# Performance work log

Measured on AMD Instinct MI355X. Metric: run time of the kernel, lower is better.

Reference implementation:

```python
import jax, jax.numpy as jnp
import numpy as np

B, C, T, H, W, E, K = 2, 256, 16, 32, 32, 4, 2


def setup_inputs() -> dict:
    key = jax.random.key(0)
    ks = jax.random.split(key, 5)
    x = jax.random.normal(ks[0], (B, C, T, H, W), dtype=jnp.float32)
    # gate: Conv3d(dim, E, 1) -> weight [E, C], bias [E]
    gate_w = jax.random.normal(ks[1], (E, C), dtype=jnp.float32) * 0.02
    gate_b = jnp.zeros((E,), dtype=jnp.float32)
    # experts_layer1: Conv3d(dim, dim*E, 1) -> weight [E*C, C], bias [E*C]
    w1 = jax.random.normal(ks[2], (E * C, C), dtype=jnp.float32) * 0.02
    b1 = jnp.zeros((E * C,), dtype=jnp.float32)
    # experts_layer2: Conv3d(dim*E, dim*E, 1, groups=E) -> per-expert [C, C]
    w2 = jax.random.normal(ks[3], (E, C, C), dtype=jnp.float32) * 0.02
    b2 = jnp.zeros((E, C), dtype=jnp.float32)
    return {"x": x, "gate_w": gate_w, "gate_b": gate_b,
            "w1": w1, "b1": b1, "w2": w2, "b2": b2}


def reference(x, gate_w, gate_b, w1, b1, w2, b2):
    # gating: 1x1x1 conv == channel contraction; logits [B,T,H,W,E]
    logits = jnp.einsum('bcthw,ec->bthwe', x, gate_w) + gate_b
    vals, idx = jax.lax.top_k(logits, K)              # [B,T,H,W,K]
    wk = jax.nn.softmax(vals, axis=-1).astype(x.dtype)
    # scatter top-k softmax weights back into E slots (zeros elsewhere)
    weights = jnp.sum(jax.nn.one_hot(idx, E, dtype=x.dtype) * wk[..., None],
                      axis=-2)                        # [B,T,H,W,E]
    # layer1 (dense 1x1x1 conv) + SiLU; output channels = E*C
    h = jax.nn.silu(jnp.einsum('bcthw,oc->bothw', x, w1)
                    + b1[None, :, None, None, None])
    h = h.reshape(B, E, C, T, H, W)
    # layer2: grouped 1x1x1 conv, one [C,C] matmul per expert
    expert_out = (jnp.einsum('becthw,eoc->beothw', h, w2)
                  + b2[None, :, :, None, None, None])  # [B,E,C,T,H,W]
    # weighted combine over experts + residual
    out = jnp.einsum('becthw,bthwe->bcthw', expert_out, weights)
    return out + x
```

## Files before the change

### kernel.cpp

```cpp
#include <hip/hip_runtime.h>
#include <hip/hip_bf16.h>


#define C_DIM 256
#define S_DIM 16384
#define E_DIM 4
#define MT 64
#define XST 264
#define OST 68
#define WFRAG_ELEMS 262144

typedef __attribute__((ext_vector_type(8))) short bf16x8;
typedef __attribute__((ext_vector_type(4))) short short4v;
typedef __attribute__((ext_vector_type(4))) float f32x4;

__device__ __forceinline__ short bfq(float f) {
  __hip_bfloat16 h = __float2bfloat16(f);
  return *(short*)&h;
}

__global__ __launch_bounds__(256) void prepack_kernel(
    const float* __restrict__ w1, const float* __restrict__ w2,
    __hip_bfloat16* __restrict__ dst)
{
  int o = blockIdx.x * 256 + threadIdx.x;
  int half = o >> 18;
  int idx = o & (WFRAG_ELEMS - 1);
  int j    = idx & 7;
  int lane = (idx >> 3) & 63;
  int kc   = (idx >> 9) & 7;
  int nt   = (idx >> 12) & 15;
  int e    = (idx >> 16) & 3;
  const float* src = half ? w2 : w1;
  int si = (e*256 + nt*16 + (lane & 15))*256 + kc*32 + (lane >> 4)*8 + j;
  dst[o] = __float2bfloat16(src[si]);
}

template<int MTC>
__device__ __forceinline__ void gemm1_sparse(
    const short* XsS, short* HsS, const short* w1e, const float* b1e,
    const unsigned char* plist_e, const float* wgtg_e,
    int wv, int r, int q)
{
  f32x4 hacc[MTC][2];
#pragma unroll
  for (int i = 0; i < MTC; ++i)
#pragma unroll
    for (int j = 0; j < 2; ++j) hacc[i][j] = (f32x4){0.f, 0.f, 0.f, 0.f};

  int aoff[MTC];
#pragma unroll
  for (int Mt = 0; Mt < MTC; ++Mt)
    aoff[Mt] = (int)plist_e[Mt*16 + r] * XST;

  bf16x8 bw[2][2];
#pragma unroll
  for (int t = 0; t < 2; ++t) bw[0][t] = *(const bf16x8*)(w1e + (t*8 + 0)*512);
#pragma unroll
  for (int kc = 0; kc < 8; ++kc) {
    if (kc < 7) {
#pragma unroll
      for (int t = 0; t < 2; ++t)
        bw[(kc+1)&1][t] = *(const bf16x8*)(w1e + (t*8 + kc + 1)*512);
    }
    bf16x8 a[MTC];
#pragma unroll
    for (int Mt = 0; Mt < MTC; ++Mt)
      a[Mt] = *(const bf16x8*)(XsS + aoff[Mt] + kc*32 + q*8);
#pragma unroll
    for (int Mt = 0; Mt < MTC; ++Mt)
#pragma unroll
      for (int t = 0; t < 2; ++t)
        hacc[Mt][t] = __builtin_amdgcn_mfma_f32_16x16x32_bf16(a[Mt], bw[kc&1][t], hacc[Mt][t], 0, 0, 0);
  }

#pragma unroll
  for (int Mt = 0; Mt < MTC; ++Mt) {
    const int g0 = Mt*16 + q*4;
    const unsigned pw = *(const unsigned*)(plist_e + g0);
    const f32x4 wg = *(const f32x4*)(wgtg_e + g0);
#pragma unroll
    for (int t = 0; t < 2; ++t) {
      const int n = wv*32 + t*16 + r;
      const float bias = b1e[n];
#pragma unroll
      for (int reg = 0; reg < 4; ++reg) {
        const int p = (pw >> (8*reg)) & 255;
        const float z = hacc[Mt][t][reg] + bias;
        const float s = __builtin_amdgcn_rcpf(1.0f + __expf(-z));
        HsS[p*XST + n] = bfq(z * s * wg[reg]);
      }
    }
  }
}

__global__ __launch_bounds__(512, 4) void moe_fused_kernel(
    const float* __restrict__ x,
    const float* __restrict__ gate_w,
    const float* __restrict__ gate_b,
    const float* __restrict__ b1,
    const float* __restrict__ b2,
    const __hip_bfloat16* __restrict__ wp,
    float* __restrict__ out)
{
  __shared__ __align__(16) char pool[256 * OST * 4];
  __shared__ float Wgt[MT * 4];
  __shared__ double GateP[512];
  __shared__ __align__(16) unsigned char plist[4][64];
  __shared__ __align__(16) float WgtG[4][64];
  __shared__ __align__(4)  unsigned char zlist[4][64];
  __shared__ int mcnt[4];

  short* XsS = (short*)pool;
  short* HsS = (short*)(pool + MT * XST * 2);
  float* Os  = (float*)pool;

  const int tid  = threadIdx.x;
  const int lane = tid & 63;
  const int wv   = tid >> 6;
  const int r    = lane & 15;
  const int q    = lane >> 4;

  const int g  = blockIdx.x;
  const int b  = g >> 8;
  const int s0 = (g & 255) * MT;
  const float* xb = x + (size_t)b * C_DIM * S_DIM + s0;

  {
    const int p4 = (tid & 15) * 4;
    const int cg = tid >> 4;
#pragma unroll
    for (int cc = 0; cc < 2; ++cc) {
      const int c0 = (cc*32 + cg) * 4;
      const float4 v0 = *(const float4*)(xb + (size_t)(c0+0)*S_DIM + p4);
      const float4 v1 = *(const float4*)(xb + (size_t)(c0+1)*S_DIM + p4);
      const float4 v2 = *(const float4*)(xb + (size_t)(c0+2)*S_DIM + p4);
      const float4 v3 = *(const float4*)(xb + (size_t)(c0+3)*S_DIM + p4);
      *(short4v*)(XsS + (p4+0)*XST + c0) = (short4v){bfq(v0.x), bfq(v1.x), bfq(v2.x), bfq(v3.x)};
      *(short4v*)(XsS + (p4+1)*XST + c0) = (short4v){bfq(v0.y), bfq(v1.y), bfq(v2.y), bfq(v3.y)};
      *(short4v*)(XsS + (p4+2)*XST + c0) = (short4v){bfq(v0.z), bfq(v1.z), bfq(v2.z), bfq(v3.z)};
      *(short4v*)(XsS + (p4+3)*XST + c0) = (short4v){bfq(v0.w), bfq(v1.w), bfq(v2.w), bfq(v3.w)};
    }
  }

  {
    const int p  = lane;
    const int e  = wv & 3;
    const int ch = wv >> 2;
    const float* gw = gate_w + e * C_DIM + ch * 128;
    const float* xr = xb + p + (size_t)(ch * 128) * S_DIM;
    double a0 = 0.0, a1 = 0.0, a2 = 0.0, a3 = 0.0;
#pragma unroll 4
    for (int c = 0; c < 128; c += 4) {
      a0 += (double)xr[(size_t)(c+0) * S_DIM] * (double)gw[c+0];
      a1 += (double)xr[(size_t)(c+1) * S_DIM] * (double)gw[c+1];
      a2 += (double)xr[(size_t)(c+2) * S_DIM] * (double)gw[c+2];
      a3 += (double)xr[(size_t)(c+3) * S_DIM] * (double)gw[c+3];
    }
    GateP[(ch*64 + p)*4 + e] = (a0 + a1) + (a2 + a3);
  }
  __syncthreads();

  if (tid < MT) {
    const int p = tid;
    float l[4];
#pragma unroll
    for (int e = 0; e < 4; ++e)
      l[e] = (float)(GateP[p*4 + e] + GateP[(64 + p)*4 + e] + (double)gate_b[e]);
    int i1 = 0; float v1 = l[0];
    if (l[1] > v1) { v1 = l[1]; i1 = 1; }
    if (l[2] > v1) { v1 = l[2]; i1 = 2; }
    if (l[3] > v1) { v1 = l[3]; i1 = 3; }
    float v2 = -3.0e38f; int i2 = 0;
    if (i1 != 0 && l[0] > v2) { v2 = l[0]; i2 = 0; }
    if (i1 != 1 && l[1] > v2) { v2 = l[1]; i2 = 1; }
    if (i1 != 2 && l[2] > v2) { v2 = l[2]; i2 = 2; }
    if (i1 != 3 && l[3] > v2) { v2 = l[3]; i2 = 3; }
    const float wA = 1.0f / (1.0f + __expf(v2 - v1));
    const float wB = 1.0f - wA;
    Wgt[p*4+0] = (i1 == 0) ? wA : ((i2 == 0) ? wB : 0.0f);
    Wgt[p*4+1] = (i1 == 1) ? wA : ((i2 == 1) ? wB : 0.0f);
    Wgt[p*4+2] = (i1 == 2) ? wA : ((i2 == 2) ? wB : 0.0f);
    Wgt[p*4+3] = (i1 == 3) ? wA : ((i2 == 3) ? wB : 0.0f);
  }
  __syncthreads();

  if (wv < 4) {
    const int e = wv;
    const int p = lane;
    const float w = Wgt[p*4 + e];
    const bool sel = (w != 0.0f);
    const unsigned long long mask = __ballot(sel);
    const int below = __popcll(mask & ((1ull << p) - 1ull));
    const int m = __popcll(mask);
    const int pad = (((m + 15) >> 4) << 4) - m;
    if (sel) {
      plist[e][below] = (unsigned char)p;
      WgtG[e][below]  = w;
    } else {
      const int zidx = p - below;
      zlist[e][zidx] = (unsigned char)p;
      if (zidx < pad) {
        plist[e][m + zidx] = (unsigned char)p;
        WgtG[e][m + zidx]  = 0.0f;
      }
    }
    if (p == 0) mcnt[e] = m;
  }
  __syncthreads();

  const short* W1P = (const short*)wp;
  const short* W2P = (const short*)wp + WFRAG_ELEMS;

  f32x4 oacc[4][2];
#pragma unroll
  for (int i = 0; i < 4; ++i)
#pragma unroll
    for (int j = 0; j < 2; ++j) oacc[i][j] = (f32x4){0.f, 0.f, 0.f, 0.f};

  for (int e = 0; e < E_DIM; ++e) {
    const int me = mcnt[e];
    const int mt = __builtin_amdgcn_readfirstlane((me + 15) >> 4);
    const short* w1e = W1P + ((e*16 + wv*2)*8)*512 + lane*8;
    const float* b1e = b1 + e*256;

    if      (mt == 2) gemm1_sparse<2>(XsS, HsS, w1e, b1e, plist[e], WgtG[e], wv, r, q);
    else if (mt == 3) gemm1_sparse<3>(XsS, HsS, w1e, b1e, plist[e], WgtG[e], wv, r, q);
    else if (mt == 4) gemm1_sparse<4>(XsS, HsS, w1e, b1e, plist[e], WgtG[e], wv, r, q);
    else if (mt == 1) gemm1_sparse<1>(XsS, HsS, w1e, b1e, plist[e], WgtG[e], wv, r, q);

    const short* w2e = W2P + ((e*16 + wv*2)*8)*512 + lane*8;
    bf16x8 cw[2][2];
#pragma unroll
    for (int t = 0; t < 2; ++t) cw[0][t] = *(const bf16x8*)(w2e + (t*8 + 0)*512);

    {
      const int zm = 64 - me;
      const bf16x8 zz = {0,0,0,0,0,0,0,0};
      for (int i = tid; i < zm*32; i += 512) {
        const int row = zlist[e][i >> 5];
        *(bf16x8*)(HsS + row*XST + (i & 31)*8) = zz;
      }
    }
    __syncthreads();

    {
#pragma unroll
      for (int kc = 0; kc < 8; ++kc) {
        if (kc < 7) {
#pragma unroll
          for (int t = 0; t < 2; ++t)
            cw[(kc+1)&1][t] = *(const bf16x8*)(w2e + (t*8 + kc + 1)*512);
        }
        bf16x8 a[4];
#pragma unroll
        for (int Mt = 0; Mt < 4; ++Mt)
          a[Mt] = *(const bf16x8*)(HsS + (Mt*16 + r)*XST + kc*32 + q*8);
#pragma unroll
        for (int Mt = 0; Mt < 4; ++Mt)
#pragma unroll
          for (int t = 0; t < 2; ++t)
            oacc[Mt][t] = __builtin_amdgcn_mfma_f32_16x16x32_bf16(a[Mt], cw[kc&1][t], oacc[Mt][t], 0, 0, 0);
      }
    }
    __syncthreads();
  }

  {
    float b2v[2][4];
#pragma unroll
    for (int t = 0; t < 2; ++t) {
      const int c = wv*32 + t*16 + r;
#pragma unroll
      for (int e = 0; e < 4; ++e) b2v[t][e] = b2[e*256 + c];
    }
#pragma unroll
    for (int Mt = 0; Mt < 4; ++Mt) {
      f32x4 wv4[4];
#pragma unroll
      for (int reg = 0; reg < 4; ++reg)
        wv4[reg] = *(const f32x4*)(&Wgt[(Mt*16 + q*4 + reg)*4]);
#pragma unroll
      for (int t = 0; t < 2; ++t) {
        f32x4 v = oacc[Mt][t];
#pragma unroll
        for (int reg = 0; reg < 4; ++reg)
          v[reg] += wv4[reg][0]*b2v[t][0] + wv4[reg][1]*b2v[t][1]
                  + wv4[reg][2]*b2v[t][2] + wv4[reg][3]*b2v[t][3];
        *(f32x4*)(Os + (size_t)(wv*32 + t*16 + r)*OST + Mt*16 + q*4) = v;
      }
    }
  }
  __syncthreads();

  {
    const int p4 = (tid & 15) * 4;
    const int cg = tid >> 4;
    float* ob = out + (size_t)b * C_DIM * S_DIM + s0;
#pragma unroll
    for (int cc = 0; cc < 8; ++cc) {
      const int c = cc*32 + cg;
      const f32x4  o  = *(const f32x4*)(Os + (size_t)c*OST + p4);
      const float4 xr = *(const float4*)(xb + (size_t)c*S_DIM + p4);
      float4 res;
      res.x = o[0] + xr.x; res.y = o[1] + xr.y;
      res.z = o[2] + xr.z; res.w = o[3] + xr.w;
      *(float4*)(ob + (size_t)c*S_DIM + p4) = res;
    }
  }
}

extern "C" void kernel_launch(void* const* d_in, const int* in_sizes, int n_in,
                              void* d_out, int out_size, void* d_ws, size_t ws_size,
                              hipStream_t stream)
{
  (void)in_sizes; (void)n_in; (void)out_size; (void)ws_size;
  const float* x      = (const float*)d_in[0];
  const float* gate_w = (const float*)d_in[1];
  const float* gate_b = (const float*)d_in[2];
  const float* w1     = (const float*)d_in[3];
  const float* b1     = (const float*)d_in[4];
  const float* w2     = (const float*)d_in[5];
  const float* b2     = (const float*)d_in[6];
  float* out = (float*)d_out;
  __hip_bfloat16* wpack = (__hip_bfloat16*)d_ws;

  prepack_kernel<<<2048, 256, 0, stream>>>(w1, w2, wpack);
  moe_fused_kernel<<<512, 512, 0, stream>>>(x, gate_w, gate_b, b1, b2, wpack, out);
}
```

Measured before the change: 136.6 us.

## Vectorize prepack, fuse x load with gate dot, and defer per-expert barrier

Result: faster. 128.2 us (-6.1%).

```diff
diff --git a/kernel.cpp b/kernel.cpp
--- a/kernel.cpp
+++ b/kernel.cpp
@@ -11,7 +11,6 @@
 #define WFRAG_ELEMS 262144
 
 typedef __attribute__((ext_vector_type(8))) short bf16x8;
-typedef __attribute__((ext_vector_type(4))) short short4v;
 typedef __attribute__((ext_vector_type(4))) float f32x4;
 
 __device__ __forceinline__ short bfq(float f) {
@@ -23,24 +22,28 @@
     const float* __restrict__ w1, const float* __restrict__ w2,
     __hip_bfloat16* __restrict__ dst)
 {
-  int o = blockIdx.x * 256 + threadIdx.x;
+  int o8 = blockIdx.x * 256 + threadIdx.x;
+  int o  = o8 << 3;
   int half = o >> 18;
-  int idx = o & (WFRAG_ELEMS - 1);
-  int j    = idx & 7;
+  int idx  = o & (WFRAG_ELEMS - 1);
   int lane = (idx >> 3) & 63;
   int kc   = (idx >> 9) & 7;
   int nt   = (idx >> 12) & 15;
   int e    = (idx >> 16) & 3;
   const float* src = half ? w2 : w1;
-  int si = (e*256 + nt*16 + (lane & 15))*256 + kc*32 + (lane >> 4)*8 + j;
-  dst[o] = __float2bfloat16(src[si]);
+  const float* s = src + (e*256 + nt*16 + (lane & 15))*256 + kc*32 + (lane >> 4)*8;
+  const float4 v0 = *(const float4*)s;
+  const float4 v1 = *(const float4*)(s + 4);
+  bf16x8 outv = {bfq(v0.x), bfq(v0.y), bfq(v0.z), bfq(v0.w),
+                 bfq(v1.x), bfq(v1.y), bfq(v1.z), bfq(v1.w)};
+  *(bf16x8*)((short*)dst + o) = outv;
 }
 
 template<int MTC>
 __device__ __forceinline__ void gemm1_sparse(
     const short* XsS, short* HsS, const short* w1e, const float* b1e,
     const unsigned char* plist_e, const float* wgtg_e,
-    int wv, int r, int q)
+    int wv, int r, int q, bool dosync)
 {
   f32x4 hacc[MTC][2];
 #pragma unroll
@@ -73,6 +76,8 @@
       for (int t = 0; t < 2; ++t)
         hacc[Mt][t] = __builtin_amdgcn_mfma_f32_16x16x32_bf16(a[Mt], bw[kc&1][t], hacc[Mt][t], 0, 0, 0);
   }
+
+  if (dosync) __syncthreads();
 
 #pragma unroll
   for (int Mt = 0; Mt < MTC; ++Mt) {
@@ -104,8 +109,7 @@
     float* __restrict__ out)
 {
   __shared__ __align__(16) char pool[256 * OST * 4];
-  __shared__ float Wgt[MT * 4];
-  __shared__ double GateP[512];
+  __shared__ __align__(16) float Wgt[MT * 4];
   __shared__ __align__(16) unsigned char plist[4][64];
   __shared__ __align__(16) float WgtG[4][64];
   __shared__ __align__(4)  unsigned char zlist[4][64];
@@ -127,61 +131,68 @@
   const float* xb = x + (size_t)b * C_DIM * S_DIM + s0;
 
   {
-    const int p4 = (tid & 15) * 4;
-    const int cg = tid >> 4;
-#pragma unroll
-    for (int cc = 0; cc < 2; ++cc) {
-      const int c0 = (cc*32 + cg) * 4;
-      const float4 v0 = *(const float4*)(xb + (size_t)(c0+0)*S_DIM + p4);
-      const float4 v1 = *(const float4*)(xb + (size_t)(c0+1)*S_DIM + p4);
-      const float4 v2 = *(const float4*)(xb + (size_t)(c0+2)*S_DIM + p4);
-      const float4 v3 = *(const float4*)(xb + (size_t)(c0+3)*S_DIM + p4);
-      *(short4v*)(XsS + (p4+0)*XST + c0) = (short4v){bfq(v0.x), bfq(v1.x), bfq(v2.x), bfq(v3.x)};
-      *(short4v*)(XsS + (p4+1)*XST + c0) = (short4v){bfq(v0.y), bfq(v1.y), bfq(v2.y), bfq(v3.y)};
-      *(short4v*)(XsS + (p4+2)*XST + c0) = (short4v){bfq(v0.z), bfq(v1.z), bfq(v2.z), bfq(v3.z)};
-      *(short4v*)(XsS + (p4+3)*XST + c0) = (short4v){bfq(v0.w), bfq(v1.w), bfq(v2.w), bfq(v3.w)};
-    }
-  }
-
-  {
     const int p  = lane;
-    const int e  = wv & 3;
-    const int ch = wv >> 2;
-    const float* gw = gate_w + e * C_DIM + ch * 128;
-    const float* xr = xb + p + (size_t)(ch * 128) * S_DIM;
-    double a0 = 0.0, a1 = 0.0, a2 = 0.0, a3 = 0.0;
-#pragma unroll 4
-    for (int c = 0; c < 128; c += 4) {
-      a0 += (double)xr[(size_t)(c+0) * S_DIM] * (double)gw[c+0];
-      a1 += (double)xr[(size_t)(c+1) * S_DIM] * (double)gw[c+1];
-      a2 += (double)xr[(size_t)(c+2) * S_DIM] * (double)gw[c+2];
-      a3 += (double)xr[(size_t)(c+3) * S_DIM] * (double)gw[c+3];
-    }
-    GateP[(ch*64 + p)*4 + e] = (a0 + a1) + (a2 + a3);
-  }
-  __syncthreads();
-
-  if (tid < MT) {
-    const int p = tid;
-    float l[4];
+    const int c0 = wv * 32;
+    float xv[32];
+#pragma unroll
+    for (int j = 0; j < 32; ++j)
+      xv[j] = xb[(size_t)(c0 + j) * S_DIM + p];
+
+    double acc[4] = {0.0, 0.0, 0.0, 0.0};
+#pragma unroll
+    for (int j = 0; j < 32; ++j) {
+      const double xd = (double)xv[j];
+      acc[0] += xd * (double)gate_w[0*256 + c0 + j];
+      acc[1] += xd * (double)gate_w[1*256 + c0 + j];
+      acc[2] += xd * (double)gate_w[2*256 + c0 + j];
+      acc[3] += xd * (double)gate_w[3*256 + c0 + j];
+    }
+
+#pragma unroll
+    for (int k = 0; k < 4; ++k) {
+      bf16x8 blk = {bfq(xv[k*8+0]), bfq(xv[k*8+1]), bfq(xv[k*8+2]), bfq(xv[k*8+3]),
+                    bfq(xv[k*8+4]), bfq(xv[k*8+5]), bfq(xv[k*8+6]), bfq(xv[k*8+7])};
+      *(bf16x8*)(XsS + p*XST + c0 + k*8) = blk;
+    }
+
+    double* GateD = (double*)HsS;
 #pragma unroll
     for (int e = 0; e < 4; ++e)
-      l[e] = (float)(GateP[p*4 + e] + GateP[(64 + p)*4 + e] + (double)gate_b[e]);
-    int i1 = 0; float v1 = l[0];
-    if (l[1] > v1) { v1 = l[1]; i1 = 1; }
-    if (l[2] > v1) { v1 = l[2]; i1 = 2; }
-    if (l[3] > v1) { v1 = l[3]; i1 = 3; }
-    float v2 = -3.0e38f; int i2 = 0;
-    if (i1 != 0 && l[0] > v2) { v2 = l[0]; i2 = 0; }
-    if (i1 != 1 && l[1] > v2) { v2 = l[1]; i2 = 1; }
-    if (i1 != 2 && l[2] > v2) { v2 = l[2]; i2 = 2; }
-    if (i1 != 3 && l[3] > v2) { v2 = l[3]; i2 = 3; }
-    const float wA = 1.0f / (1.0f + __expf(v2 - v1));
-    const float wB = 1.0f - wA;
-    Wgt[p*4+0] = (i1 == 0) ? wA : ((i2 == 0) ? wB : 0.0f);
-    Wgt[p*4+1] = (i1 == 1) ? wA : ((i2 == 1) ? wB : 0.0f);
-    Wgt[p*4+2] = (i1 == 2) ? wA : ((i2 == 2) ? wB : 0.0f);
-    Wgt[p*4+3] = (i1 == 3) ? wA : ((i2 == 3) ? wB : 0.0f);
+      GateD[(e*8 + wv)*64 + p] = acc[e];
+  }
+  __syncthreads();
+
+  if (tid < 256) {
+    const int p = tid >> 2;
+    const int e = tid & 3;
+    const double* GateD = (const double*)HsS;
+    double s = (double)gate_b[e];
+#pragma unroll
+    for (int g2 = 0; g2 < 8; ++g2) s += GateD[(e*8 + g2)*64 + p];
+    const float la = (float)s;
+    const float lb = __shfl_xor(la, 1, 64);
+    const float lc = __shfl_xor(la, 2, 64);
+    const float ld = __shfl_xor(lb, 2, 64);
+    if (e == 0) {
+      const float l0 = la, l1 = lb, l2 = lc, l3 = ld;
+      int i1 = 0; float v1 = l0;
+      if (l1 > v1) { v1 = l1; i1 = 1; }
+      if (l2 > v1) { v1 = l2; i1 = 2; }
+      if (l3 > v1) { v1 = l3; i1 = 3; }
+      float v2 = -3.0e38f; int i2 = 0;
+      if (i1 != 0 && l0 > v2) { v2 = l0; i2 = 0; }
+      if (i1 != 1 && l1 > v2) { v2 = l1; i2 = 1; }
+      if (i1 != 2 && l2 > v2) { v2 = l2; i2 = 2; }
+      if (i1 != 3 && l3 > v2) { v2 = l3; i2 = 3; }
+      const float wA = 1.0f / (1.0f + __expf(v2 - v1));
+      const float wB = 1.0f - wA;
+      f32x4 w;
+      w[0] = (i1 == 0) ? wA : ((i2 == 0) ? wB : 0.0f);
+      w[1] = (i1 == 1) ? wA : ((i2 == 1) ? wB : 0.0f);
+      w[2] = (i1 == 2) ? wA : ((i2 == 2) ? wB : 0.0f);
+      w[3] = (i1 == 3) ? wA : ((i2 == 3) ? wB : 0.0f);
+      *(f32x4*)(&Wgt[p*4]) = w;
+    }
   }
   __syncthreads();
 
@@ -223,11 +234,13 @@
     const int mt = __builtin_amdgcn_readfirstlane((me + 15) >> 4);
     const short* w1e = W1P + ((e*16 + wv*2)*8)*512 + lane*8;
     const float* b1e = b1 + e*256;
-
-    if      (mt == 2) gemm1_sparse<2>(XsS, HsS, w1e, b1e, plist[e], WgtG[e], wv, r, q);
-    else if (mt == 3) gemm1_sparse<3>(XsS, HsS, w1e, b1e, plist[e], WgtG[e], wv, r, q);
-    else if (mt == 4) gemm1_sparse<4>(XsS, HsS, w1e, b1e, plist[e], WgtG[e], wv, r, q);
-    else if (mt == 1) gemm1_sparse<1>(XsS, HsS, w1e, b1e, plist[e], WgtG[e], wv, r, q);
+    const bool dosync = (e > 0);
+
+    if      (mt == 2) gemm1_sparse<2>(XsS, HsS, w1e, b1e, plist[e], WgtG[e], wv, r, q, dosync);
+    else if (mt == 3) gemm1_sparse<3>(XsS, HsS, w1e, b1e, plist[e], WgtG[e], wv, r, q, dosync);
+    else if (mt == 4) gemm1_sparse<4>(XsS, HsS, w1e, b1e, plist[e], WgtG[e], wv, r, q, dosync);
+    else if (mt == 1) gemm1_sparse<1>(XsS, HsS, w1e, b1e, plist[e], WgtG[e], wv, r, q, dosync);
+    else { if (dosync) __syncthreads(); }
 
     const short* w2e = W2P + ((e*16 + wv*2)*8)*512 + lane*8;
     bf16x8 cw[2][2];
@@ -263,8 +276,8 @@
             oacc[Mt][t] = __builtin_amdgcn_mfma_f32_16x16x32_bf16(a[Mt], cw[kc&1][t], oacc[Mt][t], 0, 0, 0);
       }
     }
-    __syncthreads();
-  }
+  }
+  __syncthreads();
 
   {
     float b2v[2][4];
@@ -325,6 +338,6 @@
   float* out = (float*)d_out;
   __hip_bfloat16* wpack = (__hip_bfloat16*)d_ws;
 
-  prepack_kernel<<<2048, 256, 0, stream>>>(w1, w2, wpack);
+  prepack_kernel<<<256, 256, 0, stream>>>(w1, w2, wpack);
   moe_fused_kernel<<<512, 512, 0, stream>>>(x, gate_w, gate_b, b1, b2, wpack, out);
 }
```
